# Performance work log

Hardware: AMD Instinct MI355X
Metric: run time of the kernel (lower is better)

## Reference

```python
import jax, jax.numpy as jnp
import numpy as np

B, S, H, NH = 512, 128, 128, 8
F_STATIC, F_DYN = 2, 2
T_STEPS = S  # fixed decode length (CVRP demands exhausted in <= S steps)


def setup_inputs() -> dict:
    key = jax.random.key(0)
    ks = jax.random.split(key, 20)
    sc = 0.08  # xavier-ish init scale
    inp = {
        "static": jax.random.uniform(ks[0], (B, F_STATIC, S), jnp.float32),
        "dynamic": jax.random.uniform(ks[1], (B, F_DYN, S), jnp.float32),
        "distances": jax.random.uniform(ks[2], (B, S, S), jnp.float32),
        # static encoder: per-node embed + 1 MHA block
        "w_static": jax.random.normal(ks[3], (H, F_STATIC)) * sc,
        "b_static": jnp.zeros((H,), jnp.float32),
        "Wq": jax.random.normal(ks[4], (H, H)) * sc,
        "Wk": jax.random.normal(ks[5], (H, H)) * sc,
        "Wv": jax.random.normal(ks[6], (H, H)) * sc,
        "Wo": jax.random.normal(ks[7], (H, H)) * sc,
        # dynamic encoder (Conv1d k=1) and decoder-input embedding
        "w_dyn": jax.random.normal(ks[8], (H, F_DYN)) * sc,
        "w_dec_in": jax.random.normal(ks[9], (H, F_STATIC)) * sc,
        # LSTM decoder (PyTorch gate order i,f,g,o)
        "W_ih": jax.random.normal(ks[10], (4 * H, H)) * sc,
        "W_hh": jax.random.normal(ks[11], (4 * H, H)) * sc,
        "b_ih": jnp.zeros((4 * H,), jnp.float32),
        "b_hh": jnp.zeros((4 * H,), jnp.float32),
        # pointer attention v^T tanh(W1 e + W2 d + W3 h)
        "W1": jax.random.normal(ks[12], (H, H)) * sc,
        "W2": jax.random.normal(ks[13], (H, H)) * sc,
        "W3": jax.random.normal(ks[14], (H, H)) * sc,
        "v_att": jax.random.normal(ks[15], (H,)) * sc,
    }
    return inp


def reference(static, dynamic, distances, w_static, b_static, Wq, Wk, Wv, Wo,
              w_dyn, w_dec_in, W_ih, W_hh, b_ih, b_hh, W1, W2, W3, v_att):
    Bn, _, Sn = static.shape
    Hn = w_static.shape[0]
    DH = Hn // NH
    # --- encoder_static: per-node linear embed + one MHA block with residual ---
    e0 = jnp.einsum('bfs,hf->bsh', static, w_static) + b_static          # [B,S,H]
    q = (e0 @ Wq).reshape(Bn, Sn, NH, DH)
    k = (e0 @ Wk).reshape(Bn, Sn, NH, DH)
    v = (e0 @ Wv).reshape(Bn, Sn, NH, DH)
    att = jax.nn.softmax(jnp.einsum('bqhd,bkhd->bhqk', q, k) / jnp.sqrt(jnp.float32(DH)), axis=-1)
    mh = jnp.einsum('bhqk,bkhd->bqhd', att, v).reshape(Bn, Sn, Hn)
    emb = e0 + mh @ Wo                                                    # [B,S,H]
    emb_t = emb.transpose(0, 2, 1)                                        # [B,H,S]
    e_proj = jnp.einsum('hk,bks->bhs', W1, emb_t)                         # hoisted: static part of attn
    # --- initial decoder input: ones embedded (use_seperate_decoder_input_embedding) ---
    x0 = jnp.ones((Bn, F_STATIC), static.dtype) @ w_dec_in.T              # [B,H]
    h0 = jnp.zeros((Bn, Hn), static.dtype)
    c0 = jnp.zeros((Bn, Hn), static.dtype)
    base_key = jax.random.key(42)
    bidx = jnp.arange(Bn)

    def step(carry, t):
        h, c, x, dyn = carry
        # single-layer LSTM cell (PyTorch gate order i,f,g,o)
        gates = x @ W_ih.T + h @ W_hh.T + b_ih + b_hh                     # [B,4H]
        i, f, g, o = jnp.split(gates, 4, axis=-1)
        c = jax.nn.sigmoid(f) * c + jax.nn.sigmoid(i) * jnp.tanh(g)
        h = jax.nn.sigmoid(o) * jnp.tanh(c)
        # dynamic encoder (conv1d k=1) on current dynamic state
        dyn_emb = jnp.einsum('bfs,hf->bhs', dyn, w_dyn)                   # [B,H,S]
        # pointer attention
        u = jnp.tanh(e_proj + jnp.einsum('hk,bks->bhs', W2, dyn_emb) + (h @ W3.T)[:, :, None])
        scores = jnp.einsum('h,bhs->bs', v_att, u)                        # [B,S]
        logp_all = jax.nn.log_softmax(scores, axis=-1)
        # categorical sample (detached, like ptr.data.detach())
        ptr = jax.random.categorical(jax.random.fold_in(base_key, t),
                                     jax.lax.stop_gradient(logp_all))     # [B]
        logp = jnp.take_along_axis(logp_all, ptr[:, None], axis=1)[:, 0]
        # update_dynamic: zero demand (feature 1) at visited node
        dyn = dyn.at[bidx, 1, ptr].set(0.0)
        # next decoder input: embed chosen static coords
        x = jnp.take_along_axis(static, ptr[:, None, None], axis=2)[:, :, 0] @ w_dec_in.T
        return (h, c, x, dyn), (ptr, logp)

    _, (tours, tour_logp) = jax.lax.scan(step, (h0, c0, x0, dynamic), jnp.arange(T_STEPS))
    return tours.T, tour_logp.T   # [B,T], [B,T]
```

## Files before the change

### kernel.cpp

```cpp
#include <hip/hip_runtime.h>
#include <stdint.h>

__global__ void MHA_CVRP_solver_23089744183363_kernel() {}

__device__ __forceinline__ void threefry2x32(uint32_t k0, uint32_t k1,
                                             uint32_t x0, uint32_t x1,
                                             uint32_t& o0, uint32_t& o1) {
  uint32_t ks2 = k0 ^ k1 ^ 0x1BD11BDAu;
  x0 += k0; x1 += k1;
#define TF_R(r) { x0 += x1; x1 = (x1 << (r)) | (x1 >> (32 - (r))); x1 ^= x0; }
  TF_R(13) TF_R(15) TF_R(26) TF_R(6)
  x0 += k1; x1 += ks2 + 1u;
  TF_R(17) TF_R(29) TF_R(16) TF_R(24)
  x0 += ks2; x1 += k0 + 2u;
  TF_R(13) TF_R(15) TF_R(26) TF_R(6)
  x0 += k0; x1 += k1 + 3u;
  TF_R(17) TF_R(29) TF_R(16) TF_R(24)
  x0 += k1; x1 += ks2 + 4u;
  TF_R(13) TF_R(15) TF_R(26) TF_R(6)
  x0 += ks2; x1 += k0 + 5u;
#undef TF_R
  o0 = x0; o1 = x1;
}

__global__ __launch_bounds__(256) void k_att(
    const float* __restrict__ statics, const float* __restrict__ w_static,
    const float* __restrict__ b_static, const float* __restrict__ Wq,
    const float* __restrict__ Wk, const float* __restrict__ Wv,
    float* __restrict__ mh_g) {
  __shared__ __align__(16) float ws2[256];
  __shared__ __align__(16) float bss[128];
  __shared__ __align__(16) float wst[6144];
  __shared__ __align__(16) float qh[2560];
  __shared__ __align__(16) float kh[2560];
  __shared__ __align__(16) float vh[2560];
  const int tid = threadIdx.x;
  const int b = (int)blockIdx.x >> 3;
  const int head = (int)blockIdx.x & 7;

  ws2[tid] = w_static[tid];
  if (tid < 128) bss[tid] = b_static[tid];
  for (int i = tid; i < 2048; i += 256) {
    int k = i >> 4, d = i & 15;
    int so = k * 128 + head * 16 + d;
    wst[i]        = Wq[so];
    wst[2048 + i] = Wk[so];
    wst[4096 + i] = Wv[so];
  }
  __syncthreads();

  {
    const int s = tid >> 1, d0 = (tid & 1) * 8;
    const float st0 = statics[b * 256 + s];
    const float st1 = statics[b * 256 + 128 + s];
    float aq[8], ak[8], av[8];
#pragma unroll
    for (int i = 0; i < 8; ++i) { aq[i] = 0.f; ak[i] = 0.f; av[i] = 0.f; }
    for (int k = 0; k < 128; ++k) {
      float e0v = fmaf(st1, ws2[2 * k + 1], st0 * ws2[2 * k]) + bss[k];
      const float* wq = wst + k * 16 + d0;
      const float* wk = wst + 2048 + k * 16 + d0;
      const float* wv = wst + 4096 + k * 16 + d0;
#pragma unroll
      for (int l = 0; l < 8; ++l) {
        aq[l] = fmaf(e0v, wq[l], aq[l]);
        ak[l] = fmaf(e0v, wk[l], ak[l]);
        av[l] = fmaf(e0v, wv[l], av[l]);
      }
    }
    float* qd = qh + s * 20 + d0;
    float* kd = kh + s * 20 + d0;
    float* vd = vh + s * 20 + d0;
#pragma unroll
    for (int l = 0; l < 8; ++l) { qd[l] = aq[l]; kd[l] = ak[l]; vd[l] = av[l]; }
  }
  __syncthreads();

  const int rq = tid >> 2;
  const int q4 = tid & 3;
  const int j0 = q4 * 32;
  float qA[16], qB[16];
  {
    const float4* pa = (const float4*)(qh + rq * 20);
    const float4* pb = (const float4*)(qh + (rq + 64) * 20);
#pragma unroll
    for (int l = 0; l < 4; ++l) {
      float4 va = pa[l], vb = pb[l];
      qA[4 * l] = va.x; qA[4 * l + 1] = va.y; qA[4 * l + 2] = va.z; qA[4 * l + 3] = va.w;
      qB[4 * l] = vb.x; qB[4 * l + 1] = vb.y; qB[4 * l + 2] = vb.z; qB[4 * l + 3] = vb.w;
    }
  }
  float sA[32], sB[32];
#pragma unroll
  for (int j = 0; j < 32; ++j) {
    const float4* kp = (const float4*)(kh + (j0 + j) * 20);
    float4 k0 = kp[0], k1 = kp[1], k2 = kp[2], k3 = kp[3];
    float kr[16] = {k0.x, k0.y, k0.z, k0.w, k1.x, k1.y, k1.z, k1.w,
                    k2.x, k2.y, k2.z, k2.w, k3.x, k3.y, k3.z, k3.w};
    float dA = qA[0] * kr[0], dB = qB[0] * kr[0];
#pragma unroll
    for (int l = 1; l < 16; ++l) { dA = fmaf(qA[l], kr[l], dA); dB = fmaf(qB[l], kr[l], dB); }
    sA[j] = 0.25f * dA; sB[j] = 0.25f * dB;
  }
  float mA = sA[0], mB = sB[0];
#pragma unroll
  for (int j = 1; j < 32; ++j) { mA = fmaxf(mA, sA[j]); mB = fmaxf(mB, sB[j]); }
  mA = fmaxf(mA, __shfl_xor(mA, 1, 64)); mA = fmaxf(mA, __shfl_xor(mA, 2, 64));
  mB = fmaxf(mB, __shfl_xor(mB, 1, 64)); mB = fmaxf(mB, __shfl_xor(mB, 2, 64));
  float sumA = 0.f, sumB = 0.f;
#pragma unroll
  for (int j = 0; j < 32; ++j) {
    float eA = expf(sA[j] - mA); sA[j] = eA; sumA += eA;
    float eB = expf(sB[j] - mB); sB[j] = eB; sumB += eB;
  }
  sumA += __shfl_xor(sumA, 1, 64); sumA += __shfl_xor(sumA, 2, 64);
  sumB += __shfl_xor(sumB, 1, 64); sumB += __shfl_xor(sumB, 2, 64);
  const float rA = 1.0f / sumA, rB = 1.0f / sumB;
  float aA[16], aB[16];
#pragma unroll
  for (int l = 0; l < 16; ++l) { aA[l] = 0.f; aB[l] = 0.f; }
#pragma unroll
  for (int j = 0; j < 32; ++j) {
    const float4* vp = (const float4*)(vh + (j0 + j) * 20);
    float4 v0 = vp[0], v1 = vp[1], v2 = vp[2], v3 = vp[3];
    float vr[16] = {v0.x, v0.y, v0.z, v0.w, v1.x, v1.y, v1.z, v1.w,
                    v2.x, v2.y, v2.z, v2.w, v3.x, v3.y, v3.z, v3.w};
    float pA = sA[j] * rA, pB = sB[j] * rB;
#pragma unroll
    for (int l = 0; l < 16; ++l) { aA[l] = fmaf(pA, vr[l], aA[l]); aB[l] = fmaf(pB, vr[l], aB[l]); }
  }
#pragma unroll
  for (int l = 0; l < 16; ++l) {
    aA[l] += __shfl_xor(aA[l], 1, 64); aA[l] += __shfl_xor(aA[l], 2, 64);
    aB[l] += __shfl_xor(aB[l], 1, 64); aB[l] += __shfl_xor(aB[l], 2, 64);
  }
  if (q4 == 0) {
    const size_t base = (size_t)b * 16384 + head * 16;
    float4* dA = (float4*)(mh_g + base + rq * 128);
    dA[0] = make_float4(aA[0], aA[1], aA[2], aA[3]);
    dA[1] = make_float4(aA[4], aA[5], aA[6], aA[7]);
    dA[2] = make_float4(aA[8], aA[9], aA[10], aA[11]);
    dA[3] = make_float4(aA[12], aA[13], aA[14], aA[15]);
    float4* dB = (float4*)(mh_g + base + (rq + 64) * 128);
    dB[0] = make_float4(aB[0], aB[1], aB[2], aB[3]);
    dB[1] = make_float4(aB[4], aB[5], aB[6], aB[7]);
    dB[2] = make_float4(aB[8], aB[9], aB[10], aB[11]);
    dB[3] = make_float4(aB[12], aB[13], aB[14], aB[15]);
  }
}

__global__ __launch_bounds__(256) void k_out(
    const float* __restrict__ mh_g, const float* __restrict__ Wo,
    const float* __restrict__ statics, const float* __restrict__ w_static,
    const float* __restrict__ b_static, float* __restrict__ emb_g) {
  __shared__ __align__(16) float As[32 * 132];
  __shared__ __align__(16) float Bs[32 * 132];
  __shared__ __align__(16) float ws2[256];
  __shared__ __align__(16) float bss[128];
  const int tid = threadIdx.x;
  const int b = (int)blockIdx.x;
  ws2[tid] = w_static[tid];
  if (tid < 128) bss[tid] = b_static[tid];
  const int ls = tid >> 1, lk = (tid & 1) * 16;
  const int ty = tid >> 4, tx = tid & 15;
  const int lbk = tid >> 3, ljb = (tid & 7) * 16;
  float acc[8][8];
#pragma unroll
  for (int r = 0; r < 8; ++r)
#pragma unroll
    for (int c = 0; c < 8; ++c) acc[r][c] = 0.f;
  __syncthreads();
  for (int kc = 0; kc < 4; ++kc) {
#pragma unroll
    for (int j4 = 0; j4 < 4; ++j4) {
      float4 v = *(const float4*)(mh_g + (size_t)b * 16384 + ls * 128 + kc * 32 + lk + 4 * j4);
      As[(lk + 4 * j4 + 0) * 132 + ls] = v.x;
      As[(lk + 4 * j4 + 1) * 132 + ls] = v.y;
      As[(lk + 4 * j4 + 2) * 132 + ls] = v.z;
      As[(lk + 4 * j4 + 3) * 132 + ls] = v.w;
    }
    {
      const float* src = Wo + (kc * 32 + lbk) * 128 + ljb;
      float* dst = Bs + lbk * 132 + ljb;
#pragma unroll
      for (int l = 0; l < 16; ++l) dst[l] = src[l];
    }
    __syncthreads();
#pragma unroll 4
    for (int kk = 0; kk < 32; ++kk) {
      float4 a0 = *(const float4*)(As + kk * 132 + ty * 8);
      float4 a1 = *(const float4*)(As + kk * 132 + ty * 8 + 4);
      float4 b0 = *(const float4*)(Bs + kk * 132 + tx * 8);
      float4 b1 = *(const float4*)(Bs + kk * 132 + tx * 8 + 4);
      float avv[8] = {a0.x, a0.y, a0.z, a0.w, a1.x, a1.y, a1.z, a1.w};
      float bvv[8] = {b0.x, b0.y, b0.z, b0.w, b1.x, b1.y, b1.z, b1.w};
#pragma unroll
      for (int r = 0; r < 8; ++r)
#pragma unroll
        for (int c = 0; c < 8; ++c) acc[r][c] = fmaf(avv[r], bvv[c], acc[r][c]);
    }
    __syncthreads();
  }
#pragma unroll
  for (int r = 0; r < 8; ++r) {
    int row = ty * 8 + r;
    float s0 = statics[b * 256 + row];
    float s1 = statics[b * 256 + 128 + row];
    float ov[8];
#pragma unroll
    for (int c = 0; c < 8; ++c) {
      int j = tx * 8 + c;
      float e0 = fmaf(s1, ws2[2 * j + 1], s0 * ws2[2 * j]) + bss[j];
      ov[c] = e0 + acc[r][c];
    }
    float4* dst = (float4*)(emb_g + (size_t)b * 16384 + row * 128 + tx * 8);
    dst[0] = make_float4(ov[0], ov[1], ov[2], ov[3]);
    dst[1] = make_float4(ov[4], ov[5], ov[6], ov[7]);
  }
}

__global__ __launch_bounds__(256) void k_base(
    const float* __restrict__ emb_g, const float* __restrict__ W1,
    const float* __restrict__ W2, const float* __restrict__ w_dyn,
    const float* __restrict__ dynamics, float* __restrict__ baseC_g) {
  __shared__ __align__(16) float As[32 * 132];
  __shared__ __align__(16) float Bs[32 * 132];
  __shared__ __align__(16) float wd0[128];
  __shared__ __align__(16) float wd1[128];
  __shared__ __align__(16) float dy0[128];
  __shared__ __align__(16) float dy1[128];
  const int tid = threadIdx.x;
  const int b = (int)blockIdx.x;
  if (tid < 128) {
    float A0 = 0.f, A1 = 0.f;
    const float* w2r = W2 + tid * 128;
    for (int k = 0; k < 128; ++k) {
      float w = w2r[k];
      A0 = fmaf(w, w_dyn[2 * k], A0);
      A1 = fmaf(w, w_dyn[2 * k + 1], A1);
    }
    wd0[tid] = A0; wd1[tid] = A1;
    dy0[tid] = dynamics[b * 256 + tid];
    dy1[tid] = dynamics[b * 256 + 128 + tid];
  }
  const int ls = tid >> 1, lk = (tid & 1) * 16;
  const int ty = tid >> 4, tx = tid & 15;
  float acc[8][8];
#pragma unroll
  for (int r = 0; r < 8; ++r)
#pragma unroll
    for (int c = 0; c < 8; ++c) acc[r][c] = 0.f;
  __syncthreads();
  for (int kc = 0; kc < 4; ++kc) {
#pragma unroll
    for (int j4 = 0; j4 < 4; ++j4) {
      float4 v = *(const float4*)(emb_g + (size_t)b * 16384 + ls * 128 + kc * 32 + lk + 4 * j4);
      As[(lk + 4 * j4 + 0) * 132 + ls] = v.x;
      As[(lk + 4 * j4 + 1) * 132 + ls] = v.y;
      As[(lk + 4 * j4 + 2) * 132 + ls] = v.z;
      As[(lk + 4 * j4 + 3) * 132 + ls] = v.w;
    }
    {
      const float* src = W1 + ls * 128 + kc * 32 + lk;
#pragma unroll
      for (int l = 0; l < 16; ++l) Bs[(lk + l) * 132 + ls] = src[l];
    }
    __syncthreads();
#pragma unroll 4
    for (int kk = 0; kk < 32; ++kk) {
      float4 a0 = *(const float4*)(As + kk * 132 + ty * 8);
      float4 a1 = *(const float4*)(As + kk * 132 + ty * 8 + 4);
      float4 b0 = *(const float4*)(Bs + kk * 132 + tx * 8);
      float4 b1 = *(const float4*)(Bs + kk * 132 + tx * 8 + 4);
      float avv[8] = {a0.x, a0.y, a0.z, a0.w, a1.x, a1.y, a1.z, a1.w};
      float bvv[8] = {b0.x, b0.y, b0.z, b0.w, b1.x, b1.y, b1.z, b1.w};
#pragma unroll
      for (int r = 0; r < 8; ++r)
#pragma unroll
        for (int c = 0; c < 8; ++c) acc[r][c] = fmaf(avv[r], bvv[c], acc[r][c]);
    }
    __syncthreads();
  }
#pragma unroll
  for (int r = 0; r < 8; ++r) {
    int row = ty * 8 + r;
    float d0 = dy0[row], d1 = dy1[row];
    float ov[8];
#pragma unroll
    for (int c = 0; c < 8; ++c) {
      int h = tx * 8 + c;
      ov[c] = fmaf(wd1[h], d1, fmaf(wd0[h], d0, acc[r][c]));
    }
    float4* dst = (float4*)(baseC_g + (size_t)b * 16384 + row * 128 + tx * 8);
    dst[0] = make_float4(ov[0], ov[1], ov[2], ov[3]);
    dst[1] = make_float4(ov[4], ov[5], ov[6], ov[7]);
  }
}

__global__ __launch_bounds__(512, 2) void k_dec(
    const float* __restrict__ baseC_g, const float* __restrict__ statics,
    const float* __restrict__ dynamics, const float* __restrict__ W_ih,
    const float* __restrict__ W_hh, const float* __restrict__ b_ih,
    const float* __restrict__ b_hh, const float* __restrict__ w_dec_in,
    const float* __restrict__ W2, const float* __restrict__ w_dyn,
    const float* __restrict__ W3, const float* __restrict__ v_att,
    float* __restrict__ out) {
  __shared__ __align__(16) float bC0s[32 * 512];
  __shared__ __align__(16) float bC1s[32 * 512];
  __shared__ __align__(16) float hbuf0[128], hbuf1[128];
  __shared__ __align__(16) float cbuf0[128], cbuf1[128];
  __shared__ __align__(16) float gpre0[512], gpre1[512];
  __shared__ __align__(16) float hw3p0[512], hw3p1[512];
  __shared__ __align__(16) float rep0[528], rep1[528];
  __shared__ __align__(16) float vrep[528];
  __shared__ __align__(16) float scb0[128], scb1[128];
  __shared__ __align__(16) float wd1c[128];
  __shared__ __align__(16) float dyn0s[128], dyn1s[128];
  __shared__ float rmax0[2], rmax1[2], rsum0[2], rsum1[2], rval0[2], rval1[2];
  __shared__ int ridx0[2], ridx1[2];
  __shared__ float ssel0[2], ssel1[2];
  __shared__ int ptr0S, ptr1S;

  const int tid = threadIdx.x;
  const int b0 = (int)blockIdx.x * 2;
  const int b1 = b0 + 1;

  float wh[128];
  {
    const float4* src = (const float4*)(W_hh + tid * 128);
#pragma unroll
    for (int q = 0; q < 32; ++q) {
      float4 v = src[q];
      wh[4 * q] = v.x; wh[4 * q + 1] = v.y; wh[4 * q + 2] = v.z; wh[4 * q + 3] = v.w;
    }
  }
  const int uC = tid & 127, kcC = tid >> 7;
  float w3r[32];
  {
    const float4* src = (const float4*)(W3 + uC * 128 + kcC * 32);
#pragma unroll
    for (int q = 0; q < 8; ++q) {
      float4 v = src[q];
      w3r[4 * q] = v.x; w3r[4 * q + 1] = v.y; w3r[4 * q + 2] = v.z; w3r[4 * q + 3] = v.w;
    }
  }

  float a0 = 0.f, a1 = 0.f;
  {
    const float* wr = W_ih + tid * 128;
    for (int k = 0; k < 128; ++k) {
      float w = wr[k];
      a0 = fmaf(w, w_dec_in[2 * k], a0);
      a1 = fmaf(w, w_dec_in[2 * k + 1], a1);
    }
  }
  const float bsum = b_ih[tid] + b_hh[tid];

  if (tid < 128) {
    float acc1 = 0.f;
    const float* w2r = W2 + tid * 128;
    for (int k = 0; k < 128; ++k) acc1 = fmaf(w2r[k], w_dyn[2 * k + 1], acc1);
    wd1c[tid] = acc1;
    dyn0s[tid] = dynamics[b0 * 256 + 128 + tid];
    dyn1s[tid] = dynamics[b1 * 256 + 128 + tid];
    hbuf0[tid] = 0.f; cbuf0[tid] = 0.f;
    hbuf1[tid] = 0.f; cbuf1[tid] = 0.f;
    float nv = v_att[tid];
    vrep[tid] = nv; vrep[132 + tid] = nv; vrep[264 + tid] = nv; vrep[396 + tid] = nv;
  }
  const int sD = tid >> 2, qD = tid & 3;
  {
    const float4* s0 = (const float4*)(baseC_g + (size_t)b0 * 16384 + sD * 128 + qD * 32);
    const float4* s1 = (const float4*)(baseC_g + (size_t)b1 * 16384 + sD * 128 + qD * 32);
#pragma unroll
    for (int j = 0; j < 8; ++j) {
      float4 v = s0[j];
      bC0s[(4 * j + 0) * 512 + tid] = v.x;
      bC0s[(4 * j + 1) * 512 + tid] = v.y;
      bC0s[(4 * j + 2) * 512 + tid] = v.z;
      bC0s[(4 * j + 3) * 512 + tid] = v.w;
      float4 w = s1[j];
      bC1s[(4 * j + 0) * 512 + tid] = w.x;
      bC1s[(4 * j + 1) * 512 + tid] = w.y;
      bC1s[(4 * j + 2) * 512 + tid] = w.z;
      bC1s[(4 * j + 3) * 512 + tid] = w.w;
    }
  }
  __syncthreads();
  float xa0 = a0 + a1, xa1 = a0 + a1;

  for (int t = 0; t < 128; ++t) {
    uint32_t fk0, fk1;
    threefry2x32(0u, 42u, 0u, (uint32_t)t, fk0, fk1);

    {
      float acc0 = bsum + xa0;
      const float4* hp0 = (const float4*)hbuf0;
#pragma unroll
      for (int q = 0; q < 32; ++q) {
        float4 hv = hp0[q];
        acc0 = fmaf(wh[4 * q], hv.x, acc0);
        acc0 = fmaf(wh[4 * q + 1], hv.y, acc0);
        acc0 = fmaf(wh[4 * q + 2], hv.z, acc0);
        acc0 = fmaf(wh[4 * q + 3], hv.w, acc0);
      }
      gpre0[tid] = acc0;
      float acc1v = bsum + xa1;
      const float4* hp1 = (const float4*)hbuf1;
#pragma unroll
      for (int q = 0; q < 32; ++q) {
        float4 hv = hp1[q];
        acc1v = fmaf(wh[4 * q], hv.x, acc1v);
        acc1v = fmaf(wh[4 * q + 1], hv.y, acc1v);
        acc1v = fmaf(wh[4 * q + 2], hv.z, acc1v);
        acc1v = fmaf(wh[4 * q + 3], hv.w, acc1v);
      }
      gpre1[tid] = acc1v;
    }
    __syncthreads();
    if (tid < 128) {
      float gi = gpre0[tid], gf = gpre0[128 + tid], gg = gpre0[256 + tid], go = gpre0[384 + tid];
      float si = 1.f / (1.f + expf(-gi));
      float sf = 1.f / (1.f + expf(-gf));
      float so = 1.f / (1.f + expf(-go));
      float cn = sf * cbuf0[tid] + si * tanhf(gg);
      float hn = so * tanhf(cn);
      cbuf0[tid] = cn; hbuf0[tid] = hn;
    } else if (tid >= 256 && tid < 384) {
      int u = tid - 256;
      float gi = gpre1[u], gf = gpre1[128 + u], gg = gpre1[256 + u], go = gpre1[384 + u];
      float si = 1.f / (1.f + expf(-gi));
      float sf = 1.f / (1.f + expf(-gf));
      float so = 1.f / (1.f + expf(-go));
      float cn = sf * cbuf1[u] + si * tanhf(gg);
      float hn = so * tanhf(cn);
      cbuf1[u] = cn; hbuf1[u] = hn;
    }
    __syncthreads();
    {
      const float4* hp0 = (const float4*)(hbuf0 + kcC * 32);
      float p0 = 0.f;
#pragma unroll
      for (int j = 0; j < 8; ++j) {
        float4 hv = hp0[j];
        p0 = fmaf(w3r[4 * j], hv.x, p0); p0 = fmaf(w3r[4 * j + 1], hv.y, p0);
        p0 = fmaf(w3r[4 * j + 2], hv.z, p0); p0 = fmaf(w3r[4 * j + 3], hv.w, p0);
      }
      hw3p0[kcC * 128 + uC] = p0;
      const float4* hp1 = (const float4*)(hbuf1 + kcC * 32);
      float p1 = 0.f;
#pragma unroll
      for (int j = 0; j < 8; ++j) {
        float4 hv = hp1[j];
        p1 = fmaf(w3r[4 * j], hv.x, p1); p1 = fmaf(w3r[4 * j + 1], hv.y, p1);
        p1 = fmaf(w3r[4 * j + 2], hv.z, p1); p1 = fmaf(w3r[4 * j + 3], hv.w, p1);
      }
      hw3p1[kcC * 128 + uC] = p1;
    }
    __syncthreads();
    rep0[kcC * 132 + uC] =
        ((hw3p0[uC] + hw3p0[128 + uC]) + hw3p0[256 + uC]) + hw3p0[384 + uC];
    rep1[kcC * 132 + uC] =
        ((hw3p1[uC] + hw3p1[128 + uC]) + hw3p1[256 + uC]) + hw3p1[384 + uC];
    __syncthreads();
    {
      const float* vp = vrep + 164 * qD;
      const float* h0 = rep0 + 164 * qD;
      float acc = 0.f;
#pragma unroll
      for (int j = 0; j < 32; ++j)
        acc = fmaf(vp[j], tanhf(bC0s[j * 512 + tid] + h0[j]), acc);
      acc += __shfl_xor(acc, 1, 64);
      acc += __shfl_xor(acc, 2, 64);
      if (qD == 0) scb0[sD] = acc;
      const float* h1 = rep1 + 164 * qD;
      float acc1v = 0.f;
#pragma unroll
      for (int j = 0; j < 32; ++j)
        acc1v = fmaf(vp[j], tanhf(bC1s[j * 512 + tid] + h1[j]), acc1v);
      acc1v += __shfl_xor(acc1v, 1, 64);
      acc1v += __shfl_xor(acc1v, 2, 64);
      if (qD == 0) scb1[sD] = acc1v;
    }
    __syncthreads();
    const int g0 = (tid < 128);
    const int g1 = (tid >= 256 && tid < 384);
    const int lE = g0 ? tid : (tid - 256);
    float scv = 0.f, lpv = 0.f, mrow = 0.f;
    if (g0 || g1) {
      scv = g0 ? scb0[lE] : scb1[lE];
      float m = scv;
#pragma unroll
      for (int off = 32; off; off >>= 1) m = fmaxf(m, __shfl_xor(m, off, 64));
      if ((lE & 63) == 0) { if (g0) rmax0[lE >> 6] = m; else rmax1[lE >> 6] = m; }
    }
    __syncthreads();
    if (g0 || g1) {
      mrow = g0 ? fmaxf(rmax0[0], rmax0[1]) : fmaxf(rmax1[0], rmax1[1]);
      float sum = expf(scv - mrow);
#pragma unroll
      for (int off = 32; off; off >>= 1) sum += __shfl_xor(sum, off, 64);
      if ((lE & 63) == 0) { if (g0) rsum0[lE >> 6] = sum; else rsum1[lE >> 6] = sum; }
    }
    __syncthreads();
    if (g0 || g1) {
      float sum = g0 ? (rsum0[0] + rsum0[1]) : (rsum1[0] + rsum1[1]);
      lpv = (scv - mrow) - logf(sum);
      int bb = g0 ? b0 : b1;
      uint32_t j = (uint32_t)(bb * 128 + lE);
      uint32_t o0, o1;
      threefry2x32(fk0, fk1, 0u, j, o0, o1);
      uint32_t bits = o0 ^ o1;
      float f = __uint_as_float(0x3f800000u | (bits >> 9)) - 1.0f;
      float u = (f > 0.0f) ? f : 1.17549435e-38f;
      float val = lpv - logf(-logf(u));
      int idx = lE;
#pragma unroll
      for (int off = 32; off; off >>= 1) {
        float ov = __shfl_xor(val, off, 64);
        int oi = __shfl_xor(idx, off, 64);
        if (ov > val || (ov == val && oi < idx)) { val = ov; idx = oi; }
      }
      if ((lE & 63) == 0) {
        if (g0) { rval0[lE >> 6] = val; ridx0[lE >> 6] = idx; }
        else    { rval1[lE >> 6] = val; ridx1[lE >> 6] = idx; }
      }
    }
    __syncthreads();
    if (g0 || g1) {
      int p;
      if (g0) { float v0 = rval0[0], v1 = rval0[1];
                p = (v1 > v0) ? ridx0[1] : ridx0[0]; }
      else    { float v0 = rval1[0], v1 = rval1[1];
                p = (v1 > v0) ? ridx1[1] : ridx1[0]; }
      p &= 127;
      int bb = g0 ? b0 : b1;
      if (lE == 0) {
        if (g0) ptr0S = p; else ptr1S = p;
        out[bb * 128 + t] = (float)p;
      }
      if (lE == p) {
        out[65536 + bb * 128 + t] = lpv;
        if (g0) { ssel0[0] = statics[bb * 256 + p]; ssel0[1] = statics[bb * 256 + 128 + p]; }
        else    { ssel1[0] = statics[bb * 256 + p]; ssel1[1] = statics[bb * 256 + 128 + p]; }
      }
    }
    __syncthreads();
    {
      int p0 = ptr0S, p1 = ptr1S;
      if (sD == p0) {
        float d1 = dyn0s[p0];
#pragma unroll
        for (int i = 0; i < 32; ++i)
          bC0s[i * 512 + tid] = fmaf(-wd1c[qD * 32 + i], d1, bC0s[i * 512 + tid]);
      }
      if (sD == p1) {
        float d1 = dyn1s[p1];
#pragma unroll
        for (int i = 0; i < 32; ++i)
          bC1s[i * 512 + tid] = fmaf(-wd1c[qD * 32 + i], d1, bC1s[i * 512 + tid]);
      }
      xa0 = fmaf(a0, ssel0[0], a1 * ssel0[1]);
      xa1 = fmaf(a0, ssel1[0], a1 * ssel1[1]);
    }
    __syncthreads();
    if (tid == 0) { dyn0s[ptr0S] = 0.f; dyn1s[ptr1S] = 0.f; }
  }
}

extern "C" __attribute__((visibility("default")))
void kernel_launch(void* const* d_in, const int* in_sizes, int n_in,
                   void* d_out, int out_size, void* d_ws, size_t ws_size,
                   hipStream_t stream) {
  (void)hipGetLastError();
  (void)in_sizes; (void)n_in; (void)out_size; (void)ws_size;

  const float* statics  = (const float*)d_in[0];
  const float* dynamics = (const float*)d_in[1];
  const float* w_static = (const float*)d_in[3];
  const float* b_static = (const float*)d_in[4];
  const float* Wq  = (const float*)d_in[5];
  const float* Wk  = (const float*)d_in[6];
  const float* Wv  = (const float*)d_in[7];
  const float* Wo  = (const float*)d_in[8];
  const float* w_dyn    = (const float*)d_in[9];
  const float* w_dec_in = (const float*)d_in[10];
  const float* W_ih = (const float*)d_in[11];
  const float* W_hh = (const float*)d_in[12];
  const float* b_ih = (const float*)d_in[13];
  const float* b_hh = (const float*)d_in[14];
  const float* W1   = (const float*)d_in[15];
  const float* W2   = (const float*)d_in[16];
  const float* W3   = (const float*)d_in[17];
  const float* v_att = (const float*)d_in[18];
  float* wsA = (float*)d_ws;
  float* wsB = wsA + 8388608;
  float* outp = (float*)d_out;

  k_att<<<dim3(4096), dim3(256), 0, stream>>>(
      statics, w_static, b_static, Wq, Wk, Wv, wsB);
  k_out<<<dim3(512), dim3(256), 0, stream>>>(
      wsB, Wo, statics, w_static, b_static, wsA);
  k_base<<<dim3(512), dim3(256), 0, stream>>>(
      wsA, W1, W2, w_dyn, dynamics, wsB);
  k_dec<<<dim3(256), dim3(512), 0, stream>>>(
      wsB, statics, dynamics, W_ih, W_hh, b_ih, b_hh, w_dec_in,
      W2, w_dyn, W3, v_att, outp);
}
```

Measured before the change: 2.063 ms.

## Do softmax and sampling in one wavefront per batch and interleave the paired batches

The per-step log-softmax, Gumbel sampling and argmax now run inside a single 64-lane wavefront per batch element, with each lane handling two nodes. This removes the shared-memory partial reductions and several block-wide barriers per decode step. The two batch elements' LSTM, W3 and tanh-score loops are interleaved to expose more instruction-level parallelism. Static coordinates are cached in shared memory, and the dyn zeroing moves into the update block, dropping the trailing barrier. The cost is more serial work inside one wavefront, while the other waves sit idle.

Result: slower. 3.221 ms (+56.1%).

```diff
diff --git a/kernel.cpp b/kernel.cpp
--- a/kernel.cpp
+++ b/kernel.cpp
@@ -316,8 +316,7 @@
   __shared__ __align__(16) float scb0[128], scb1[128];
   __shared__ __align__(16) float wd1c[128];
   __shared__ __align__(16) float dyn0s[128], dyn1s[128];
-  __shared__ float rmax0[2], rmax1[2], rsum0[2], rsum1[2], rval0[2], rval1[2];
-  __shared__ int ridx0[2], ridx1[2];
+  __shared__ __align__(16) float sst0[256], sst1[256];
   __shared__ float ssel0[2], ssel1[2];
   __shared__ int ptr0S, ptr1S;
 
@@ -368,6 +367,10 @@
     float nv = v_att[tid];
     vrep[tid] = nv; vrep[132 + tid] = nv; vrep[264 + tid] = nv; vrep[396 + tid] = nv;
   }
+  if (tid < 256) {
+    sst0[tid] = statics[b0 * 256 + tid];
+    sst1[tid] = statics[b1 * 256 + tid];
+  }
   const int sD = tid >> 2, qD = tid & 3;
   {
     const float4* s0 = (const float4*)(baseC_g + (size_t)b0 * 16384 + sD * 128 + qD * 32);
@@ -395,7 +398,9 @@
 
     {
       float acc0 = bsum + xa0;
+      float acc1v = bsum + xa1;
       const float4* hp0 = (const float4*)hbuf0;
+      const float4* hp1 = (const float4*)hbuf1;
 #pragma unroll
       for (int q = 0; q < 32; ++q) {
         float4 hv = hp0[q];
@@ -403,18 +408,13 @@
         acc0 = fmaf(wh[4 * q + 1], hv.y, acc0);
         acc0 = fmaf(wh[4 * q + 2], hv.z, acc0);
         acc0 = fmaf(wh[4 * q + 3], hv.w, acc0);
+        float4 hw = hp1[q];
+        acc1v = fmaf(wh[4 * q], hw.x, acc1v);
+        acc1v = fmaf(wh[4 * q + 1], hw.y, acc1v);
+        acc1v = fmaf(wh[4 * q + 2], hw.z, acc1v);
+        acc1v = fmaf(wh[4 * q + 3], hw.w, acc1v);
       }
       gpre0[tid] = acc0;
-      float acc1v = bsum + xa1;
-      const float4* hp1 = (const float4*)hbuf1;
-#pragma unroll
-      for (int q = 0; q < 32; ++q) {
-        float4 hv = hp1[q];
-        acc1v = fmaf(wh[4 * q], hv.x, acc1v);
-        acc1v = fmaf(wh[4 * q + 1], hv.y, acc1v);
-        acc1v = fmaf(wh[4 * q + 2], hv.z, acc1v);
-        acc1v = fmaf(wh[4 * q + 3], hv.w, acc1v);
-      }
       gpre1[tid] = acc1v;
     }
     __syncthreads();
@@ -439,22 +439,18 @@
     __syncthreads();
     {
       const float4* hp0 = (const float4*)(hbuf0 + kcC * 32);
-      float p0 = 0.f;
+      const float4* hp1 = (const float4*)(hbuf1 + kcC * 32);
+      float p0 = 0.f, p1 = 0.f;
 #pragma unroll
       for (int j = 0; j < 8; ++j) {
         float4 hv = hp0[j];
         p0 = fmaf(w3r[4 * j], hv.x, p0); p0 = fmaf(w3r[4 * j + 1], hv.y, p0);
         p0 = fmaf(w3r[4 * j + 2], hv.z, p0); p0 = fmaf(w3r[4 * j + 3], hv.w, p0);
+        float4 hw = hp1[j];
+        p1 = fmaf(w3r[4 * j], hw.x, p1); p1 = fmaf(w3r[4 * j + 1], hw.y, p1);
+        p1 = fmaf(w3r[4 * j + 2], hw.z, p1); p1 = fmaf(w3r[4 * j + 3], hw.w, p1);
       }
       hw3p0[kcC * 128 + uC] = p0;
-      const float4* hp1 = (const float4*)(hbuf1 + kcC * 32);
-      float p1 = 0.f;
-#pragma unroll
-      for (int j = 0; j < 8; ++j) {
-        float4 hv = hp1[j];
-        p1 = fmaf(w3r[4 * j], hv.x, p1); p1 = fmaf(w3r[4 * j + 1], hv.y, p1);
-        p1 = fmaf(w3r[4 * j + 2], hv.z, p1); p1 = fmaf(w3r[4 * j + 3], hv.w, p1);
-      }
       hw3p1[kcC * 128 + uC] = p1;
     }
     __syncthreads();
@@ -466,83 +462,82 @@
     {
       const float* vp = vrep + 164 * qD;
       const float* h0 = rep0 + 164 * qD;
-      float acc = 0.f;
-#pragma unroll
-      for (int j = 0; j < 32; ++j)
-        acc = fmaf(vp[j], tanhf(bC0s[j * 512 + tid] + h0[j]), acc);
+      const float* h1 = rep1 + 164 * qD;
+      float acc = 0.f, acc1v = 0.f;
+#pragma unroll
+      for (int j = 0; j < 32; ++j) {
+        acc   = fmaf(vp[j], tanhf(bC0s[j * 512 + tid] + h0[j]), acc);
+        acc1v = fmaf(vp[j], tanhf(bC1s[j * 512 + tid] + h1[j]), acc1v);
+      }
       acc += __shfl_xor(acc, 1, 64);
       acc += __shfl_xor(acc, 2, 64);
-      if (qD == 0) scb0[sD] = acc;
-      const float* h1 = rep1 + 164 * qD;
-      float acc1v = 0.f;
-#pragma unroll
-      for (int j = 0; j < 32; ++j)
-        acc1v = fmaf(vp[j], tanhf(bC1s[j * 512 + tid] + h1[j]), acc1v);
       acc1v += __shfl_xor(acc1v, 1, 64);
       acc1v += __shfl_xor(acc1v, 2, 64);
-      if (qD == 0) scb1[sD] = acc1v;
-    }
-    __syncthreads();
-    const int g0 = (tid < 128);
-    const int g1 = (tid >= 256 && tid < 384);
-    const int lE = g0 ? tid : (tid - 256);
-    float scv = 0.f, lpv = 0.f, mrow = 0.f;
-    if (g0 || g1) {
-      scv = g0 ? scb0[lE] : scb1[lE];
-      float m = scv;
-#pragma unroll
-      for (int off = 32; off; off >>= 1) m = fmaxf(m, __shfl_xor(m, off, 64));
-      if ((lE & 63) == 0) { if (g0) rmax0[lE >> 6] = m; else rmax1[lE >> 6] = m; }
-    }
-    __syncthreads();
-    if (g0 || g1) {
-      mrow = g0 ? fmaxf(rmax0[0], rmax0[1]) : fmaxf(rmax1[0], rmax1[1]);
-      float sum = expf(scv - mrow);
-#pragma unroll
-      for (int off = 32; off; off >>= 1) sum += __shfl_xor(sum, off, 64);
-      if ((lE & 63) == 0) { if (g0) rsum0[lE >> 6] = sum; else rsum1[lE >> 6] = sum; }
-    }
-    __syncthreads();
-    if (g0 || g1) {
-      float sum = g0 ? (rsum0[0] + rsum0[1]) : (rsum1[0] + rsum1[1]);
-      lpv = (scv - mrow) - logf(sum);
-      int bb = g0 ? b0 : b1;
-      uint32_t j = (uint32_t)(bb * 128 + lE);
-      uint32_t o0, o1;
-      threefry2x32(fk0, fk1, 0u, j, o0, o1);
-      uint32_t bits = o0 ^ o1;
-      float f = __uint_as_float(0x3f800000u | (bits >> 9)) - 1.0f;
-      float u = (f > 0.0f) ? f : 1.17549435e-38f;
-      float val = lpv - logf(-logf(u));
-      int idx = lE;
-#pragma unroll
-      for (int off = 32; off; off >>= 1) {
-        float ov = __shfl_xor(val, off, 64);
-        int oi = __shfl_xor(idx, off, 64);
-        if (ov > val || (ov == val && oi < idx)) { val = ov; idx = oi; }
-      }
-      if ((lE & 63) == 0) {
-        if (g0) { rval0[lE >> 6] = val; ridx0[lE >> 6] = idx; }
-        else    { rval1[lE >> 6] = val; ridx1[lE >> 6] = idx; }
-      }
-    }
-    __syncthreads();
-    if (g0 || g1) {
-      int p;
-      if (g0) { float v0 = rval0[0], v1 = rval0[1];
-                p = (v1 > v0) ? ridx0[1] : ridx0[0]; }
-      else    { float v0 = rval1[0], v1 = rval1[1];
-                p = (v1 > v0) ? ridx1[1] : ridx1[0]; }
-      p &= 127;
-      int bb = g0 ? b0 : b1;
-      if (lE == 0) {
-        if (g0) ptr0S = p; else ptr1S = p;
-        out[bb * 128 + t] = (float)p;
-      }
-      if (lE == p) {
-        out[65536 + bb * 128 + t] = lpv;
-        if (g0) { ssel0[0] = statics[bb * 256 + p]; ssel0[1] = statics[bb * 256 + 128 + p]; }
-        else    { ssel1[0] = statics[bb * 256 + p]; ssel1[1] = statics[bb * 256 + 128 + p]; }
+      if (qD == 0) { scb0[sD] = acc; scb1[sD] = acc1v; }
+    }
+    __syncthreads();
+    {
+      const int we = tid >> 6;
+      if (we == 0 || we == 4) {
+        const int l = tid & 63;
+        const bool gA = (we == 0);
+        const float* scb = gA ? scb0 : scb1;
+        const int bb = gA ? b0 : b1;
+        float sa = scb[l], sb = scb[64 + l];
+        float ma = sa, mb = sb;
+#pragma unroll
+        for (int off = 32; off; off >>= 1) {
+          ma = fmaxf(ma, __shfl_xor(ma, off, 64));
+          mb = fmaxf(mb, __shfl_xor(mb, off, 64));
+        }
+        float mrow = fmaxf(ma, mb);
+        float ra = expf(sa - mrow), rb = expf(sb - mrow);
+#pragma unroll
+        for (int off = 32; off; off >>= 1) {
+          ra += __shfl_xor(ra, off, 64);
+          rb += __shfl_xor(rb, off, 64);
+        }
+        float lsum = logf(ra + rb);
+        float lpa = (sa - mrow) - lsum;
+        float lpb = (sb - mrow) - lsum;
+        uint32_t o0, o1;
+        threefry2x32(fk0, fk1, 0u, (uint32_t)(bb * 128 + l), o0, o1);
+        uint32_t bits = o0 ^ o1;
+        float fa = __uint_as_float(0x3f800000u | (bits >> 9)) - 1.0f;
+        float ua = (fa > 0.0f) ? fa : 1.17549435e-38f;
+        float va = lpa - logf(-logf(ua));
+        threefry2x32(fk0, fk1, 0u, (uint32_t)(bb * 128 + 64 + l), o0, o1);
+        bits = o0 ^ o1;
+        float fb = __uint_as_float(0x3f800000u | (bits >> 9)) - 1.0f;
+        float ub = (fb > 0.0f) ? fb : 1.17549435e-38f;
+        float vb = lpb - logf(-logf(ub));
+        int ia = l, ib = 64 + l;
+#pragma unroll
+        for (int off = 32; off; off >>= 1) {
+          float ov = __shfl_xor(va, off, 64); int oi = __shfl_xor(ia, off, 64);
+          if (ov > va || (ov == va && oi < ia)) { va = ov; ia = oi; }
+          float ow = __shfl_xor(vb, off, 64); int oj = __shfl_xor(ib, off, 64);
+          if (ow > vb || (ow == vb && oj < ib)) { vb = ow; ib = oj; }
+        }
+        int p = (vb > va) ? ib : ia;
+        p &= 127;
+        if (l == 0) {
+          if (gA) ptr0S = p; else ptr1S = p;
+          out[bb * 128 + t] = (float)p;
+        }
+        const float* sst = gA ? sst0 : sst1;
+        if (l == p) {
+          out[65536 + bb * 128 + t] = lpa;
+          float s0v = sst[p], s1v = sst[128 + p];
+          if (gA) { ssel0[0] = s0v; ssel0[1] = s1v; }
+          else    { ssel1[0] = s0v; ssel1[1] = s1v; }
+        }
+        if (l + 64 == p) {
+          out[65536 + bb * 128 + t] = lpb;
+          float s0v = sst[p], s1v = sst[128 + p];
+          if (gA) { ssel0[0] = s0v; ssel0[1] = s1v; }
+          else    { ssel1[0] = s0v; ssel1[1] = s1v; }
+        }
       }
     }
     __syncthreads();
@@ -553,18 +548,18 @@
 #pragma unroll
         for (int i = 0; i < 32; ++i)
           bC0s[i * 512 + tid] = fmaf(-wd1c[qD * 32 + i], d1, bC0s[i * 512 + tid]);
+        if (qD == 0) dyn0s[p0] = 0.f;
       }
       if (sD == p1) {
         float d1 = dyn1s[p1];
 #pragma unroll
         for (int i = 0; i < 32; ++i)
           bC1s[i * 512 + tid] = fmaf(-wd1c[qD * 32 + i], d1, bC1s[i * 512 + tid]);
+        if (qD == 0) dyn1s[p1] = 0.f;
       }
       xa0 = fmaf(a0, ssel0[0], a1 * ssel0[1]);
       xa1 = fmaf(a0, ssel1[0], a1 * ssel1[1]);
     }
-    __syncthreads();
-    if (tid == 0) { dyn0s[ptr0S] = 0.f; dyn1s[ptr1S] = 0.f; }
   }
 }
 
```
